# Kernel optimization log

Measured on AMD Instinct MI355X. Metric: run time of the kernel, lower is better.

## Reference

```python
import jax, jax.numpy as jnp
import numpy as np

HEADS = 8
DIM_HEAD = 64
SCALE = DIM_HEAD ** -0.5


def setup_inputs() -> dict:
    key = jax.random.key(0)
    ks = jax.random.split(key, 8)
    B, Nq, Dq = 4, 2048, 512
    Nk, Dc = 1024, 768
    inner = HEADS * DIM_HEAD  # 512
    x = jax.random.normal(ks[0], (B, Nq, Dq), dtype=jnp.float32)
    context = jax.random.normal(ks[1], (B, Nk, Dc), dtype=jnp.float32)
    # Linear weights stored [in, out]; y = x @ W (+ b)
    Wq = jax.random.normal(ks[2], (Dq, inner), dtype=jnp.float32) / np.sqrt(Dq)
    Wk = jax.random.normal(ks[3], (Dc, inner), dtype=jnp.float32) / np.sqrt(Dc)
    Wv = jax.random.normal(ks[4], (Dc, inner), dtype=jnp.float32) / np.sqrt(Dc)
    Wo = jax.random.normal(ks[5], (inner, Dq), dtype=jnp.float32) / np.sqrt(inner)
    bo = jax.random.normal(ks[6], (Dq,), dtype=jnp.float32) * 0.01
    return {"x": x, "context": context, "Wq": Wq, "Wk": Wk, "Wv": Wv, "Wo": Wo, "bo": bo}


def reference(x, context, Wq, Wk, Wv, Wo, bo):
    B, Nq, _ = x.shape
    Nk = context.shape[1]
    # projections
    q = x @ Wq          # [B, Nq, h*d]
    k = context @ Wk    # [B, Nk, h*d]
    v = context @ Wv    # [B, Nk, h*d]
    # split heads: b n (h d) -> b h n d
    q = q.reshape(B, Nq, HEADS, DIM_HEAD).transpose(0, 2, 1, 3)
    k = k.reshape(B, Nk, HEADS, DIM_HEAD).transpose(0, 2, 1, 3)
    v = v.reshape(B, Nk, HEADS, DIM_HEAD).transpose(0, 2, 1, 3)
    # fp32 QK^T (ATTN_PRECISION == 'fp32' path)
    sim = jnp.einsum('bhid,bhjd->bhij', q.astype(jnp.float32), k.astype(jnp.float32)) * SCALE
    attn = jax.nn.softmax(sim, axis=-1)
    out = jnp.einsum('bhij,bhjd->bhid', attn, v)  # [B, h, Nq, d]
    out = out.transpose(0, 2, 1, 3).reshape(B, Nq, HEADS * DIM_HEAD)
    return out @ Wo + bo  # dropout=0 -> identity
```

## Files before the change

kernel.cpp:

```cpp
#include <hip/hip_runtime.h>
#include <cstddef>
#include <cstdint>

typedef __attribute__((ext_vector_type(8))) short bf16x8;
typedef __attribute__((ext_vector_type(4))) float f32x4;

static __device__ __forceinline__ short f2bf(float f) {
    union { float f; unsigned u; } x;
    x.f = f;
    unsigned r = (x.u + 0x7FFFu + ((x.u >> 16) & 1u)) >> 16;
    return (short)r;
}

typedef __attribute__((address_space(3))) unsigned lds_u;
typedef const __attribute__((address_space(1))) unsigned glb_u;
static __device__ __forceinline__ void gld_lds16(const void* g, void* l) {
    __builtin_amdgcn_global_load_lds((glb_u*)g, (lds_u*)l, 16, 0, 0);
}

__global__ __launch_bounds__(256) void prep_kernel(
    const float* __restrict__ x, const float* __restrict__ c,
    short* __restrict__ xb, short* __restrict__ cb,
    const float* __restrict__ Wq, const float* __restrict__ Wk,
    const float* __restrict__ Wv, const float* __restrict__ Wo,
    short* __restrict__ wqT, short* __restrict__ wkvT, short* __restrict__ woT)
{
    __shared__ float T[32][33];
    const int bid = blockIdx.x;
    const int tid = threadIdx.x;
    if (bid < 7168) {
        int i = bid * 256 + tid;
        const float* src; short* dst; int off;
        if (i < 1048576) { src = x; dst = xb; off = i; }
        else { src = c; dst = cb; off = i - 1048576; }
        float4 v = ((const float4*)src)[off];
        ushort4 w;
        w.x = (unsigned short)f2bf(v.x); w.y = (unsigned short)f2bf(v.y);
        w.z = (unsigned short)f2bf(v.z); w.w = (unsigned short)f2bf(v.w);
        ((ushort4*)dst)[off] = w;
        return;
    }
    const int w0 = bid - 7168;
    const int z = w0 / 384, rem = w0 % 384;
    const int yt = rem >> 4, xt = rem & 15;
    const float* src; short* dst; int R;
    if (z == 0)      { src = Wq; dst = wqT;  R = 512; }
    else if (z == 1) { src = Wk; dst = wkvT; R = 768; }
    else if (z == 2) { src = Wv; dst = wkvT + (size_t)512 * 768; R = 768; }
    else             { src = Wo; dst = woT;  R = 512; }
    if (yt * 32 >= R) return;
    {
        int r = tid >> 3, c4 = (tid & 7) * 4;
        float4 v = *(const float4*)&src[(size_t)(yt * 32 + r) * 512 + xt * 32 + c4];
        T[r][c4] = v.x; T[r][c4 + 1] = v.y; T[r][c4 + 2] = v.z; T[r][c4 + 3] = v.w;
    }
    __syncthreads();
    {
        int cc = tid >> 3, r4 = (tid & 7) * 4;
        ushort4 w;
        w.x = (unsigned short)f2bf(T[r4][cc]);     w.y = (unsigned short)f2bf(T[r4 + 1][cc]);
        w.z = (unsigned short)f2bf(T[r4 + 2][cc]); w.w = (unsigned short)f2bf(T[r4 + 3][cc]);
        *(ushort4*)&dst[(size_t)(xt * 32 + cc) * R + yt * 32 + r4] = w;
    }
}

static __device__ __forceinline__ void gemm_core(
    const short* __restrict__ A, const short* __restrict__ BT, int K,
    int bm, int bn, short* As, short* Bs, f32x4 acc[4][4])
{
    const int tid  = threadIdx.x;
    const int lane = tid & 63;
    const int wave = tid >> 6;
    const int lm   = lane & 15;
    const int quad = lane >> 4;
    const int wm = (wave >> 1) * 64;
    const int wn = (wave & 1) * 64;
    const int c = tid >> 7, r = tid & 127;

    const short* Ag = &A[(size_t)(bm + r) * K + c * 8];
    const short* Bg = &BT[(size_t)(bn + r) * K + c * 8];

    gld_lds16(Ag,      &As[tid * 8]);
    gld_lds16(Ag + 16, &As[(tid + 256) * 8]);
    gld_lds16(Bg,      &Bs[tid * 8]);
    gld_lds16(Bg + 16, &Bs[(tid + 256) * 8]);
    Ag += 32; Bg += 32;
    gld_lds16(Ag,      &As[4096 + tid * 8]);
    gld_lds16(Ag + 16, &As[4096 + (tid + 256) * 8]);
    gld_lds16(Bg,      &Bs[4096 + tid * 8]);
    gld_lds16(Bg + 16, &Bs[4096 + (tid + 256) * 8]);
    Ag += 32; Bg += 32;

    const int NT = K >> 5;
    int ocur = 0;
    int onxt = 2 * 4096;
    for (int t = 0; t < NT; ++t) {
        if (t < NT - 1) asm volatile("s_waitcnt vmcnt(4)" ::: "memory");
        else            asm volatile("s_waitcnt vmcnt(0)" ::: "memory");
        __builtin_amdgcn_s_barrier();
        __builtin_amdgcn_sched_barrier(0);
        if (t < NT - 2) {
            gld_lds16(Ag,      &As[onxt + tid * 8]);
            gld_lds16(Ag + 16, &As[onxt + (tid + 256) * 8]);
            gld_lds16(Bg,      &Bs[onxt + tid * 8]);
            gld_lds16(Bg + 16, &Bs[onxt + (tid + 256) * 8]);
            Ag += 32; Bg += 32;
        }
        const short* Ac = As + ocur;
        const short* Bc = Bs + ocur;
        bf16x8 af[4], bfr[4];
        #pragma unroll
        for (int i = 0; i < 4; ++i)
            af[i] = *(const bf16x8*)&Ac[(quad * 128 + wm + i * 16 + lm) * 8];
        #pragma unroll
        for (int j = 0; j < 4; ++j)
            bfr[j] = *(const bf16x8*)&Bc[(quad * 128 + wn + j * 16 + lm) * 8];
        __builtin_amdgcn_s_setprio(1);
        #pragma unroll
        for (int i = 0; i < 4; ++i)
            #pragma unroll
            for (int j = 0; j < 4; ++j)
                acc[i][j] = __builtin_amdgcn_mfma_f32_16x16x32_bf16(
                    af[i], bfr[j], acc[i][j], 0, 0, 0);
        __builtin_amdgcn_s_setprio(0);
        ocur += 4096; if (ocur == 12288) ocur = 0;
        onxt += 4096; if (onxt == 12288) onxt = 0;
    }
}

__global__ __launch_bounds__(256) void qkv_kernel(
    const short* __restrict__ xb, const short* __restrict__ cb,
    const short* __restrict__ wqT, const short* __restrict__ wkvT,
    short* __restrict__ qb, short* __restrict__ kvb, short* __restrict__ vT)
{
    __shared__ short As[3 * 4096];
    __shared__ short Bs[3 * 4096];
    const int L = (blockIdx.x & 7) * 64 + (blockIdx.x >> 3);
    const short *A, *BT; int K, bm, bn;
    if (L < 256) { A = xb; BT = wqT;  K = 512; bm = (L >> 2) * 128; bn = (L & 3) * 128; }
    else { int b2 = L - 256; A = cb; BT = wkvT; K = 768;
           bm = (b2 >> 3) * 128; bn = (b2 & 7) * 128; }

    f32x4 acc[4][4] = {};
    gemm_core(A, BT, K, bm, bn, As, Bs, acc);

    const int lane = threadIdx.x & 63, wave = threadIdx.x >> 6;
    const int lm = lane & 15, quad = lane >> 4;
    const int wm = (wave >> 1) * 64, wn = (wave & 1) * 64;
    if (L < 256) {
        #pragma unroll
        for (int j = 0; j < 4; ++j) {
            int col = bn + wn + j * 16 + lm;
            #pragma unroll
            for (int i = 0; i < 4; ++i) {
                int row0 = bm + wm + i * 16 + quad * 4;
                #pragma unroll
                for (int r = 0; r < 4; ++r)
                    qb[(size_t)(row0 + r) * 512 + col] = f2bf(acc[i][j][r] * 0.18033688f);
            }
        }
    } else if (bn < 512) {
        #pragma unroll
        for (int j = 0; j < 4; ++j) {
            int col = bn + wn + j * 16 + lm;
            #pragma unroll
            for (int i = 0; i < 4; ++i) {
                int row0 = bm + wm + i * 16 + quad * 4;
                #pragma unroll
                for (int r = 0; r < 4; ++r)
                    kvb[(size_t)(row0 + r) * 1024 + col] = f2bf(acc[i][j][r]);
            }
        }
    } else {
        const int bq = bm >> 10;
        const int nbase = (bm & 1023) + wm;
        #pragma unroll
        for (int j = 0; j < 4; ++j) {
            int dimp = bn + wn + j * 16 + lm - 512;
            short* drow = &vT[((size_t)(bq * 512 + dimp)) * 1024];
            #pragma unroll
            for (int i = 0; i < 4; ++i) {
                int n0 = nbase + i * 16 + quad * 4;
                int nl = n0 & 63;
                int g  = ((nl >> 5) << 2) | ((nl >> 2) & 3);
                int p  = (n0 & ~63) | (g << 3) | (((nl >> 4) & 1) << 2);
                ushort4 w;
                w.x = (unsigned short)f2bf(acc[i][j][0]);
                w.y = (unsigned short)f2bf(acc[i][j][1]);
                w.z = (unsigned short)f2bf(acc[i][j][2]);
                w.w = (unsigned short)f2bf(acc[i][j][3]);
                *(ushort4*)&drow[p] = w;
            }
        }
    }
}

__global__ __launch_bounds__(256) void ogemm_kernel(
    const short* __restrict__ ob, const short* __restrict__ woT,
    const float* __restrict__ bias, float* __restrict__ out)
{
    __shared__ short As[3 * 4096];
    __shared__ short Bs[3 * 4096];
    const int L = (blockIdx.x & 7) * 32 + (blockIdx.x >> 3);
    const int bm = (L >> 2) * 128, bn = (L & 3) * 128;

    f32x4 acc[4][4] = {};
    gemm_core(ob, woT, 512, bm, bn, As, Bs, acc);

    const int lane = threadIdx.x & 63, wave = threadIdx.x >> 6;
    const int lm = lane & 15, quad = lane >> 4;
    const int wm = (wave >> 1) * 64, wn = (wave & 1) * 64;
    #pragma unroll
    for (int j = 0; j < 4; ++j) {
        int col = bn + wn + j * 16 + lm;
        float bv = bias[col];
        #pragma unroll
        for (int i = 0; i < 4; ++i) {
            int row0 = bm + wm + i * 16 + quad * 4;
            #pragma unroll
            for (int r = 0; r < 4; ++r)
                out[(size_t)(row0 + r) * 512 + col] = acc[i][j][r] + bv;
        }
    }
}

__global__ __launch_bounds__(256) void attn_kernel(
    const short* __restrict__ q, const short* __restrict__ k,
    const short* __restrict__ vT, short* __restrict__ o)
{
    __shared__ short Ks[2 * 8192];
    __shared__ short Vs[2 * 8192];

    const int tid  = threadIdx.x;
    const int lane = tid & 63;
    const int wave = tid >> 6;
    const int lm   = lane & 15;
    const int quad = lane >> 4;

    const int bid = blockIdx.x;
    const int xcdq = bid >> 3;
    const int hb = (bid & 7) + ((xcdq >> 4) << 3);
    const int qt = xcdq & 15;
    const int h = hb & 7, b = hb >> 3;

    const size_t qrow0 = (size_t)b * 2048 + qt * 128;
    const size_t krow0 = (size_t)b * 1024;
    const int hcol = h * 64;
    const size_t vrow0 = ((size_t)b * 8 + h) * 64;

    const int rk = tid & 127, ck = tid >> 7;
    const int dv = tid & 63,  nv = tid >> 6;
    const short* kg = &k[(krow0 + rk) * 1024 + hcol + ck * 8];
    const short* vg = &vT[(vrow0 + dv) * 1024 + nv * 8];

    #pragma unroll
    for (int c = 0; c < 4; ++c)
        gld_lds16(kg + c * 16, &Ks[((ck + 2 * c) * 128 + rk) * 8]);
    #pragma unroll
    for (int c = 0; c < 4; ++c)
        gld_lds16(vg + c * 32, &Vs[((nv + 4 * c) * 64 + dv) * 8]);
    kg += 128 * 1024; vg += 128;

    const short* qrow0p = &q[(qrow0 + wave * 32 + lm) * 512 + hcol];
    const short* qrow1p = qrow0p + 16 * 512;
    bf16x8 qf00 = *(const bf16x8*)&qrow0p[quad * 8];
    bf16x8 qf01 = *(const bf16x8*)&qrow0p[32 + quad * 8];
    bf16x8 qf10 = *(const bf16x8*)&qrow1p[quad * 8];
    bf16x8 qf11 = *(const bf16x8*)&qrow1p[32 + quad * 8];
    asm volatile("" :: "v"(qf00), "v"(qf01), "v"(qf10), "v"(qf11));

    f32x4 oacc[2][4] = {};
    float lsum[2] = {0.0f, 0.0f};
    const int frk = (quad * 128 + lm) * 8;
    const int frv = (quad * 64 + lm) * 8;

    for (int t = 0; t < 8; ++t) {
        asm volatile("s_waitcnt vmcnt(0)" ::: "memory");
        __builtin_amdgcn_s_barrier();
        __builtin_amdgcn_sched_barrier(0);
        const short* Kc = &Ks[(t & 1) * 8192];
        const short* Vc = &Vs[(t & 1) * 8192];
        if (t < 7) {
            short* Kn = &Ks[((t & 1) ^ 1) * 8192];
            short* Vn = &Vs[((t & 1) ^ 1) * 8192];
            #pragma unroll
            for (int c = 0; c < 4; ++c)
                gld_lds16(kg + c * 16, &Kn[((ck + 2 * c) * 128 + rk) * 8]);
            #pragma unroll
            for (int c = 0; c < 4; ++c)
                gld_lds16(vg + c * 32, &Vn[((nv + 4 * c) * 64 + dv) * 8]);
            kg += 128 * 1024; vg += 128;
        }

        f32x4 s0[8], s1[8];
        #pragma unroll
        for (int j = 0; j < 8; ++j) { s0[j] = (f32x4){}; s1[j] = (f32x4){}; }
        __builtin_amdgcn_s_setprio(1);
        #pragma unroll
        for (int j = 0; j < 8; ++j) {
            bf16x8 kf0 = *(const bf16x8*)&Kc[frk + j * 128];
            bf16x8 kf1 = *(const bf16x8*)&Kc[frk + 4096 + j * 128];
            s0[j] = __builtin_amdgcn_mfma_f32_16x16x32_bf16(kf0, qf00, s0[j], 0, 0, 0);
            s1[j] = __builtin_amdgcn_mfma_f32_16x16x32_bf16(kf0, qf10, s1[j], 0, 0, 0);
            s0[j] = __builtin_amdgcn_mfma_f32_16x16x32_bf16(kf1, qf01, s0[j], 0, 0, 0);
            s1[j] = __builtin_amdgcn_mfma_f32_16x16x32_bf16(kf1, qf11, s1[j], 0, 0, 0);
        }
        __builtin_amdgcn_s_setprio(0);

        union { unsigned u[4]; bf16x8 v; } pf0[4], pf1[4];
        #pragma unroll
        for (int j = 0; j < 8; ++j) {
            #pragma unroll
            for (int rp = 0; rp < 2; ++rp) {
                float a0 = __builtin_amdgcn_exp2f(s0[j][2 * rp]);
                float a1 = __builtin_amdgcn_exp2f(s0[j][2 * rp + 1]);
                float b0 = __builtin_amdgcn_exp2f(s1[j][2 * rp]);
                float b1 = __builtin_amdgcn_exp2f(s1[j][2 * rp + 1]);
                lsum[0] += a0 + a1;
                lsum[1] += b0 + b1;
                unsigned pa, pb;
                asm("v_cvt_pk_bf16_f32 %0, %1, %2" : "=v"(pa) : "v"(a0), "v"(a1));
                asm("v_cvt_pk_bf16_f32 %0, %1, %2" : "=v"(pb) : "v"(b0), "v"(b1));
                pf0[j >> 1].u[(j & 1) * 2 + rp] = pa;
                pf1[j >> 1].u[(j & 1) * 2 + rp] = pb;
            }
        }

        __builtin_amdgcn_s_setprio(1);
        #pragma unroll
        for (int jd = 0; jd < 4; ++jd) {
            #pragma unroll
            for (int s = 0; s < 4; ++s) {
                bf16x8 vf = *(const bf16x8*)&Vc[frv + s * 2048 + jd * 128];
                oacc[0][jd] = __builtin_amdgcn_mfma_f32_16x16x32_bf16(pf0[s].v, vf, oacc[0][jd], 0, 0, 0);
                oacc[1][jd] = __builtin_amdgcn_mfma_f32_16x16x32_bf16(pf1[s].v, vf, oacc[1][jd], 0, 0, 0);
            }
        }
        __builtin_amdgcn_s_setprio(0);
    }

    #pragma unroll
    for (int g = 0; g < 2; ++g) {
        float s = lsum[g];
        s += __shfl_xor(s, 16);
        s += __shfl_xor(s, 32);
        const float inv = 1.0f / s;
        float invr[4];
        #pragma unroll
        for (int r = 0; r < 4; ++r)
            invr[r] = __shfl(inv, quad * 20 + r);
        #pragma unroll
        for (int j = 0; j < 4; ++j) {
            int col = hcol + j * 16 + lm;
            #pragma unroll
            for (int r = 0; r < 4; ++r) {
                size_t row = qrow0 + wave * 32 + g * 16 + quad * 4 + r;
                o[row * 512 + col] = f2bf(oacc[g][j][r] * invr[r]);
            }
        }
    }
}

extern "C" void kernel_launch(void* const* d_in, const int* in_sizes, int n_in,
                              void* d_out, int out_size, void* d_ws, size_t ws_size,
                              hipStream_t stream)
{
    const float* x   = (const float*)d_in[0];
    const float* ctx = (const float*)d_in[1];
    const float* Wq  = (const float*)d_in[2];
    const float* Wk  = (const float*)d_in[3];
    const float* Wv  = (const float*)d_in[4];
    const float* Wo  = (const float*)d_in[5];
    const float* bo  = (const float*)d_in[6];

    char* ws = (char*)d_ws;
    short* xb   = (short*)(ws);
    short* cb   = (short*)(ws + (8u << 20));
    short* wqT  = (short*)(ws + (14u << 20));
    short* wkvT = (short*)(ws + (14u << 20) + (512u << 10));
    short* woT  = (short*)(ws + (16u << 20));
    short* qb   = (short*)(ws + (16u << 20) + (512u << 10));
    short* kvb  = (short*)(ws + (24u << 20) + (512u << 10));
    short* vT   = (short*)(ws + (33u << 20));
    short* ob   = xb;

    prep_kernel<<<8704, 256, 0, stream>>>(x, ctx, xb, cb, Wq, Wk, Wv, Wo, wqT, wkvT, woT);
    qkv_kernel<<<512, 256, 0, stream>>>(xb, cb, wqT, wkvT, qb, kvb, vT);
    attn_kernel<<<512, 256, 0, stream>>>(qb, kvb, vT, ob);
    ogemm_kernel<<<256, 256, 0, stream>>>(ob, woT, bo, (float*)d_out);
}
```

Before: 164.9 us.

## Fuse four kernels into one persistent kernel with atomic grid barriers

Replaces the prep, QKV-projection, attention and output-GEMM launches with a single 512-block kernel. The stages are separated by a software grid barrier built on an atomic counter, which is reset by a memset before launch. The goal is to remove launch overhead and the tail gaps between kernels. In exchange it needs all 512 blocks co-resident (launch_bounds 256,2 and 64KB of LDS), adds spin-wait costs, and has the prep stage loop inside each block.

```diff
diff --git a/kernel.cpp b/kernel.cpp
--- a/kernel.cpp
+++ b/kernel.cpp
@@ -18,50 +18,16 @@
     __builtin_amdgcn_global_load_lds((glb_u*)g, (lds_u*)l, 16, 0, 0);
 }
 
-__global__ __launch_bounds__(256) void prep_kernel(
-    const float* __restrict__ x, const float* __restrict__ c,
-    short* __restrict__ xb, short* __restrict__ cb,
-    const float* __restrict__ Wq, const float* __restrict__ Wk,
-    const float* __restrict__ Wv, const float* __restrict__ Wo,
-    short* __restrict__ wqT, short* __restrict__ wkvT, short* __restrict__ woT)
-{
-    __shared__ float T[32][33];
-    const int bid = blockIdx.x;
-    const int tid = threadIdx.x;
-    if (bid < 7168) {
-        int i = bid * 256 + tid;
-        const float* src; short* dst; int off;
-        if (i < 1048576) { src = x; dst = xb; off = i; }
-        else { src = c; dst = cb; off = i - 1048576; }
-        float4 v = ((const float4*)src)[off];
-        ushort4 w;
-        w.x = (unsigned short)f2bf(v.x); w.y = (unsigned short)f2bf(v.y);
-        w.z = (unsigned short)f2bf(v.z); w.w = (unsigned short)f2bf(v.w);
-        ((ushort4*)dst)[off] = w;
-        return;
-    }
-    const int w0 = bid - 7168;
-    const int z = w0 / 384, rem = w0 % 384;
-    const int yt = rem >> 4, xt = rem & 15;
-    const float* src; short* dst; int R;
-    if (z == 0)      { src = Wq; dst = wqT;  R = 512; }
-    else if (z == 1) { src = Wk; dst = wkvT; R = 768; }
-    else if (z == 2) { src = Wv; dst = wkvT + (size_t)512 * 768; R = 768; }
-    else             { src = Wo; dst = woT;  R = 512; }
-    if (yt * 32 >= R) return;
-    {
-        int r = tid >> 3, c4 = (tid & 7) * 4;
-        float4 v = *(const float4*)&src[(size_t)(yt * 32 + r) * 512 + xt * 32 + c4];
-        T[r][c4] = v.x; T[r][c4 + 1] = v.y; T[r][c4 + 2] = v.z; T[r][c4 + 3] = v.w;
-    }
+static __device__ __forceinline__ void gbar(unsigned* ctr, unsigned target) {
+    asm volatile("s_waitcnt vmcnt(0) lgkmcnt(0)" ::: "memory");
+    __threadfence();
     __syncthreads();
-    {
-        int cc = tid >> 3, r4 = (tid & 7) * 4;
-        ushort4 w;
-        w.x = (unsigned short)f2bf(T[r4][cc]);     w.y = (unsigned short)f2bf(T[r4 + 1][cc]);
-        w.z = (unsigned short)f2bf(T[r4 + 2][cc]); w.w = (unsigned short)f2bf(T[r4 + 3][cc]);
-        *(ushort4*)&dst[(size_t)(xt * 32 + cc) * R + yt * 32 + r4] = w;
-    }
+    if (threadIdx.x == 0) {
+        atomicAdd(ctr, 1u);
+        while (atomicAdd(ctr, 0u) < target) __builtin_amdgcn_s_sleep(8);
+    }
+    __syncthreads();
+    __threadfence();
 }
 
 static __device__ __forceinline__ void gemm_core(
@@ -128,234 +94,282 @@
     }
 }
 
-__global__ __launch_bounds__(256) void qkv_kernel(
-    const short* __restrict__ xb, const short* __restrict__ cb,
-    const short* __restrict__ wqT, const short* __restrict__ wkvT,
-    short* __restrict__ qb, short* __restrict__ kvb, short* __restrict__ vT)
+__global__ __launch_bounds__(256, 2) void mega_kernel(
+    const float* __restrict__ x, const float* __restrict__ ctx,
+    const float* __restrict__ Wq, const float* __restrict__ Wk,
+    const float* __restrict__ Wv, const float* __restrict__ Wo,
+    const float* __restrict__ bo,
+    short* __restrict__ xb, short* __restrict__ cb,
+    short* __restrict__ wqT, short* __restrict__ wkvT, short* __restrict__ woT,
+    short* __restrict__ qb, short* __restrict__ kvb, short* __restrict__ vT,
+    short* __restrict__ ob, float* __restrict__ out, unsigned* __restrict__ ctr)
 {
-    __shared__ short As[3 * 4096];
-    __shared__ short Bs[3 * 4096];
-    const int L = (blockIdx.x & 7) * 64 + (blockIdx.x >> 3);
-    const short *A, *BT; int K, bm, bn;
-    if (L < 256) { A = xb; BT = wqT;  K = 512; bm = (L >> 2) * 128; bn = (L & 3) * 128; }
-    else { int b2 = L - 256; A = cb; BT = wkvT; K = 768;
-           bm = (b2 >> 3) * 128; bn = (b2 & 7) * 128; }
-
-    f32x4 acc[4][4] = {};
-    gemm_core(A, BT, K, bm, bn, As, Bs, acc);
-
-    const int lane = threadIdx.x & 63, wave = threadIdx.x >> 6;
-    const int lm = lane & 15, quad = lane >> 4;
-    const int wm = (wave >> 1) * 64, wn = (wave & 1) * 64;
-    if (L < 256) {
+    __shared__ __align__(16) char SMEM[65536];
+    const int bid = blockIdx.x;
+    const int tid = threadIdx.x;
+
+    {
+        #pragma unroll 1
+        for (int it = 0; it < 14; ++it) {
+            int i = (bid + it * 512) * 256 + tid;
+            const float* src; short* dst; int off;
+            if (i < 1048576) { src = x; dst = xb; off = i; }
+            else { src = ctx; dst = cb; off = i - 1048576; }
+            float4 v = ((const float4*)src)[off];
+            ushort4 w;
+            w.x = (unsigned short)f2bf(v.x); w.y = (unsigned short)f2bf(v.y);
+            w.z = (unsigned short)f2bf(v.z); w.w = (unsigned short)f2bf(v.w);
+            ((ushort4*)dst)[off] = w;
+        }
+        float (*T)[33] = (float(*)[33])SMEM;
+        #pragma unroll 1
+        for (int it = 0; it < 3; ++it) {
+            int w0 = bid + it * 512;
+            int z = w0 / 384, rem = w0 % 384;
+            int yt = rem >> 4, xt = rem & 15;
+            const float* src; short* dst; int R;
+            if (z == 0)      { src = Wq; dst = wqT;  R = 512; }
+            else if (z == 1) { src = Wk; dst = wkvT; R = 768; }
+            else if (z == 2) { src = Wv; dst = wkvT + (size_t)512 * 768; R = 768; }
+            else             { src = Wo; dst = woT;  R = 512; }
+            const bool act = (yt * 32 < R);
+            if (act) {
+                int r = tid >> 3, c4 = (tid & 7) * 4;
+                float4 v = *(const float4*)&src[(size_t)(yt * 32 + r) * 512 + xt * 32 + c4];
+                T[r][c4] = v.x; T[r][c4 + 1] = v.y; T[r][c4 + 2] = v.z; T[r][c4 + 3] = v.w;
+            }
+            __syncthreads();
+            if (act) {
+                int cc = tid >> 3, r4 = (tid & 7) * 4;
+                ushort4 w;
+                w.x = (unsigned short)f2bf(T[r4][cc]);     w.y = (unsigned short)f2bf(T[r4 + 1][cc]);
+                w.z = (unsigned short)f2bf(T[r4 + 2][cc]); w.w = (unsigned short)f2bf(T[r4 + 3][cc]);
+                *(ushort4*)&dst[(size_t)(xt * 32 + cc) * R + yt * 32 + r4] = w;
+            }
+            __syncthreads();
+        }
+    }
+    gbar(ctr, 512);
+
+    {
+        short* As = (short*)SMEM;
+        short* Bs = (short*)(SMEM + 24576);
+        const int L = (bid & 7) * 64 + (bid >> 3);
+        const short *A, *BT; int K, bm, bn;
+        if (L < 256) { A = xb; BT = wqT;  K = 512; bm = (L >> 2) * 128; bn = (L & 3) * 128; }
+        else { int b2 = L - 256; A = cb; BT = wkvT; K = 768;
+               bm = (b2 >> 3) * 128; bn = (b2 & 7) * 128; }
+
+        f32x4 acc[4][4] = {};
+        gemm_core(A, BT, K, bm, bn, As, Bs, acc);
+
+        const int lane = tid & 63, wave = tid >> 6;
+        const int lm = lane & 15, quad = lane >> 4;
+        const int wm = (wave >> 1) * 64, wn = (wave & 1) * 64;
+        if (L < 256) {
+            #pragma unroll
+            for (int j = 0; j < 4; ++j) {
+                int col = bn + wn + j * 16 + lm;
+                #pragma unroll
+                for (int i = 0; i < 4; ++i) {
+                    int row0 = bm + wm + i * 16 + quad * 4;
+                    #pragma unroll
+                    for (int r = 0; r < 4; ++r)
+                        qb[(size_t)(row0 + r) * 512 + col] = f2bf(acc[i][j][r] * 0.18033688f);
+                }
+            }
+        } else if (bn < 512) {
+            #pragma unroll
+            for (int j = 0; j < 4; ++j) {
+                int col = bn + wn + j * 16 + lm;
+                #pragma unroll
+                for (int i = 0; i < 4; ++i) {
+                    int row0 = bm + wm + i * 16 + quad * 4;
+                    #pragma unroll
+                    for (int r = 0; r < 4; ++r)
+                        kvb[(size_t)(row0 + r) * 1024 + col] = f2bf(acc[i][j][r]);
+                }
+            }
+        } else {
+            const int bq = bm >> 10;
+            const int nbase = (bm & 1023) + wm;
+            #pragma unroll
+            for (int j = 0; j < 4; ++j) {
+                int dimp = bn + wn + j * 16 + lm - 512;
+                short* drow = &vT[((size_t)(bq * 512 + dimp)) * 1024];
+                #pragma unroll
+                for (int i = 0; i < 4; ++i) {
+                    int n0 = nbase + i * 16 + quad * 4;
+                    int nl = n0 & 63;
+                    int g  = ((nl >> 5) << 2) | ((nl >> 2) & 3);
+                    int p  = (n0 & ~63) | (g << 3) | (((nl >> 4) & 1) << 2);
+                    ushort4 w;
+                    w.x = (unsigned short)f2bf(acc[i][j][0]);
+                    w.y = (unsigned short)f2bf(acc[i][j][1]);
+                    w.z = (unsigned short)f2bf(acc[i][j][2]);
+                    w.w = (unsigned short)f2bf(acc[i][j][3]);
+                    *(ushort4*)&drow[p] = w;
+                }
+            }
+        }
+    }
+    gbar(ctr, 1024);
+
+    {
+        short* Ks = (short*)SMEM;
+        short* Vs = (short*)(SMEM + 32768);
+        const int lane = tid & 63;
+        const int wave = tid >> 6;
+        const int lm   = lane & 15;
+        const int quad = lane >> 4;
+
+        const int xcdq = bid >> 3;
+        const int hb = (bid & 7) + ((xcdq >> 4) << 3);
+        const int qt = xcdq & 15;
+        const int h = hb & 7, b = hb >> 3;
+
+        const size_t qrow0 = (size_t)b * 2048 + qt * 128;
+        const size_t krow0 = (size_t)b * 1024;
+        const int hcol = h * 64;
+        const size_t vrow0 = ((size_t)b * 8 + h) * 64;
+
+        const int rk = tid & 127, ck = tid >> 7;
+        const int dv = tid & 63,  nv = tid >> 6;
+        const short* kg = &kvb[(krow0 + rk) * 1024 + hcol + ck * 8];
+        const short* vg = &vT[(vrow0 + dv) * 1024 + nv * 8];
+
+        #pragma unroll
+        for (int c = 0; c < 4; ++c)
+            gld_lds16(kg + c * 16, &Ks[((ck + 2 * c) * 128 + rk) * 8]);
+        #pragma unroll
+        for (int c = 0; c < 4; ++c)
+            gld_lds16(vg + c * 32, &Vs[((nv + 4 * c) * 64 + dv) * 8]);
+        kg += 128 * 1024; vg += 128;
+
+        const short* qrow0p = &qb[(qrow0 + wave * 32 + lm) * 512 + hcol];
+        const short* qrow1p = qrow0p + 16 * 512;
+        bf16x8 qf00 = *(const bf16x8*)&qrow0p[quad * 8];
+        bf16x8 qf01 = *(const bf16x8*)&qrow0p[32 + quad * 8];
+        bf16x8 qf10 = *(const bf16x8*)&qrow1p[quad * 8];
+        bf16x8 qf11 = *(const bf16x8*)&qrow1p[32 + quad * 8];
+        asm volatile("" :: "v"(qf00), "v"(qf01), "v"(qf10), "v"(qf11));
+
+        f32x4 oacc[2][4] = {};
+        float lsum[2] = {0.0f, 0.0f};
+        const int frk = (quad * 128 + lm) * 8;
+        const int frv = (quad * 64 + lm) * 8;
+
+        for (int t = 0; t < 8; ++t) {
+            asm volatile("s_waitcnt vmcnt(0)" ::: "memory");
+            __builtin_amdgcn_s_barrier();
+            __builtin_amdgcn_sched_barrier(0);
+            const short* Kc = &Ks[(t & 1) * 8192];
+            const short* Vc = &Vs[(t & 1) * 8192];
+            if (t < 7) {
+                short* Kn = &Ks[((t & 1) ^ 1) * 8192];
+                short* Vn = &Vs[((t & 1) ^ 1) * 8192];
+                #pragma unroll
+                for (int c = 0; c < 4; ++c)
+                    gld_lds16(kg + c * 16, &Kn[((ck + 2 * c) * 128 + rk) * 8]);
+                #pragma unroll
+                for (int c = 0; c < 4; ++c)
+                    gld_lds16(vg + c * 32, &Vn[((nv + 4 * c) * 64 + dv) * 8]);
+                kg += 128 * 1024; vg += 128;
+            }
+
+            f32x4 s0[8], s1[8];
+            #pragma unroll
+            for (int j = 0; j < 8; ++j) { s0[j] = (f32x4){}; s1[j] = (f32x4){}; }
+            __builtin_amdgcn_s_setprio(1);
+            #pragma unroll
+            for (int j = 0; j < 8; ++j) {
+                bf16x8 kf0 = *(const bf16x8*)&Kc[frk + j * 128];
+                bf16x8 kf1 = *(const bf16x8*)&Kc[frk + 4096 + j * 128];
+                s0[j] = __builtin_amdgcn_mfma_f32_16x16x32_bf16(kf0, qf00, s0[j], 0, 0, 0);
+                s1[j] = __builtin_amdgcn_mfma_f32_16x16x32_bf16(kf0, qf10, s1[j], 0, 0, 0);
+                s0[j] = __builtin_amdgcn_mfma_f32_16x16x32_bf16(kf1, qf01, s0[j], 0, 0, 0);
+                s1[j] = __builtin_amdgcn_mfma_f32_16x16x32_bf16(kf1, qf11, s1[j], 0, 0, 0);
+            }
+            __builtin_amdgcn_s_setprio(0);
+
+            union { unsigned u[4]; bf16x8 v; } pf0[4], pf1[4];
+            #pragma unroll
+            for (int j = 0; j < 8; ++j) {
+                #pragma unroll
+                for (int rp = 0; rp < 2; ++rp) {
+                    float a0 = __builtin_amdgcn_exp2f(s0[j][2 * rp]);
+                    float a1 = __builtin_amdgcn_exp2f(s0[j][2 * rp + 1]);
+                    float b0 = __builtin_amdgcn_exp2f(s1[j][2 * rp]);
+                    float b1 = __builtin_amdgcn_exp2f(s1[j][2 * rp + 1]);
+                    lsum[0] += a0 + a1;
+                    lsum[1] += b0 + b1;
+                    unsigned pa, pb;
+                    asm("v_cvt_pk_bf16_f32 %0, %1, %2" : "=v"(pa) : "v"(a0), "v"(a1));
+                    asm("v_cvt_pk_bf16_f32 %0, %1, %2" : "=v"(pb) : "v"(b0), "v"(b1));
+                    pf0[j >> 1].u[(j & 1) * 2 + rp] = pa;
+                    pf1[j >> 1].u[(j & 1) * 2 + rp] = pb;
+                }
+            }
+
+            __builtin_amdgcn_s_setprio(1);
+            #pragma unroll
+            for (int jd = 0; jd < 4; ++jd) {
+                #pragma unroll
+                for (int s = 0; s < 4; ++s) {
+                    bf16x8 vf = *(const bf16x8*)&Vc[frv + s * 2048 + jd * 128];
+                    oacc[0][jd] = __builtin_amdgcn_mfma_f32_16x16x32_bf16(pf0[s].v, vf, oacc[0][jd], 0, 0, 0);
+                    oacc[1][jd] = __builtin_amdgcn_mfma_f32_16x16x32_bf16(pf1[s].v, vf, oacc[1][jd], 0, 0, 0);
+                }
+            }
+            __builtin_amdgcn_s_setprio(0);
+        }
+
+        #pragma unroll
+        for (int g = 0; g < 2; ++g) {
+            float s = lsum[g];
+            s += __shfl_xor(s, 16);
+            s += __shfl_xor(s, 32);
+            const float inv = 1.0f / s;
+            float invr[4];
+            #pragma unroll
+            for (int r = 0; r < 4; ++r)
+                invr[r] = __shfl(inv, quad * 20 + r);
+            #pragma unroll
+            for (int j = 0; j < 4; ++j) {
+                int col = hcol + j * 16 + lm;
+                #pragma unroll
+                for (int r = 0; r < 4; ++r) {
+                    size_t row = qrow0 + wave * 32 + g * 16 + quad * 4 + r;
+                    ob[row * 512 + col] = f2bf(oacc[g][j][r] * invr[r]);
+                }
+            }
+        }
+    }
+    gbar(ctr, 1536);
+
+    if (bid >= 256) return;
+    {
+        short* As = (short*)SMEM;
+        short* Bs = (short*)(SMEM + 24576);
+        const int L = (bid & 7) * 32 + (bid >> 3);
+        const int bm = (L >> 2) * 128, bn = (L & 3) * 128;
+
+        f32x4 acc[4][4] = {};
+        gemm_core(ob, woT, 512, bm, bn, As, Bs, acc);
+
+        const int lane = tid & 63, wave = tid >> 6;
+        const int lm = lane & 15, quad = lane >> 4;
+        const int wm = (wave >> 1) * 64, wn = (wave & 1) * 64;
         #pragma unroll
         for (int j = 0; j < 4; ++j) {
             int col = bn + wn + j * 16 + lm;
+            float bv = bo[col];
             #pragma unroll
             for (int i = 0; i < 4; ++i) {
                 int row0 = bm + wm + i * 16 + quad * 4;
                 #pragma unroll
                 for (int r = 0; r < 4; ++r)
-                    qb[(size_t)(row0 + r) * 512 + col] = f2bf(acc[i][j][r] * 0.18033688f);
-            }
-        }
-    } else if (bn < 512) {
-        #pragma unroll
-        for (int j = 0; j < 4; ++j) {
-            int col = bn + wn + j * 16 + lm;
-            #pragma unroll
-            for (int i = 0; i < 4; ++i) {
-                int row0 = bm + wm + i * 16 + quad * 4;
-                #pragma unroll
-                for (int r = 0; r < 4; ++r)
-                    kvb[(size_t)(row0 + r) * 1024 + col] = f2bf(acc[i][j][r]);
-            }
-        }
-    } else {
-        const int bq = bm >> 10;
-        const int nbase = (bm & 1023) + wm;
-        #pragma unroll
-        for (int j = 0; j < 4; ++j) {
-            int dimp = bn + wn + j * 16 + lm - 512;
-            short* drow = &vT[((size_t)(bq * 512 + dimp)) * 1024];
-            #pragma unroll
-            for (int i = 0; i < 4; ++i) {
-                int n0 = nbase + i * 16 + quad * 4;
-                int nl = n0 & 63;
-                int g  = ((nl >> 5) << 2) | ((nl >> 2) & 3);
-                int p  = (n0 & ~63) | (g << 3) | (((nl >> 4) & 1) << 2);
-                ushort4 w;
-                w.x = (unsigned short)f2bf(acc[i][j][0]);
-                w.y = (unsigned short)f2bf(acc[i][j][1]);
-                w.z = (unsigned short)f2bf(acc[i][j][2]);
-                w.w = (unsigned short)f2bf(acc[i][j][3]);
-                *(ushort4*)&drow[p] = w;
-            }
-        }
-    }
-}
-
-__global__ __launch_bounds__(256) void ogemm_kernel(
-    const short* __restrict__ ob, const short* __restrict__ woT,
-    const float* __restrict__ bias, float* __restrict__ out)
-{
-    __shared__ short As[3 * 4096];
-    __shared__ short Bs[3 * 4096];
-    const int L = (blockIdx.x & 7) * 32 + (blockIdx.x >> 3);
-    const int bm = (L >> 2) * 128, bn = (L & 3) * 128;
-
-    f32x4 acc[4][4] = {};
-    gemm_core(ob, woT, 512, bm, bn, As, Bs, acc);
-
-    const int lane = threadIdx.x & 63, wave = threadIdx.x >> 6;
-    const int lm = lane & 15, quad = lane >> 4;
-    const int wm = (wave >> 1) * 64, wn = (wave & 1) * 64;
-    #pragma unroll
-    for (int j = 0; j < 4; ++j) {
-        int col = bn + wn + j * 16 + lm;
-        float bv = bias[col];
-        #pragma unroll
-        for (int i = 0; i < 4; ++i) {
-            int row0 = bm + wm + i * 16 + quad * 4;
-            #pragma unroll
-            for (int r = 0; r < 4; ++r)
-                out[(size_t)(row0 + r) * 512 + col] = acc[i][j][r] + bv;
-        }
-    }
-}
-
-__global__ __launch_bounds__(256) void attn_kernel(
-    const short* __restrict__ q, const short* __restrict__ k,
-    const short* __restrict__ vT, short* __restrict__ o)
-{
-    __shared__ short Ks[2 * 8192];
-    __shared__ short Vs[2 * 8192];
-
-    const int tid  = threadIdx.x;
-    const int lane = tid & 63;
-    const int wave = tid >> 6;
-    const int lm   = lane & 15;
-    const int quad = lane >> 4;
-
-    const int bid = blockIdx.x;
-    const int xcdq = bid >> 3;
-    const int hb = (bid & 7) + ((xcdq >> 4) << 3);
-    const int qt = xcdq & 15;
-    const int h = hb & 7, b = hb >> 3;
-
-    const size_t qrow0 = (size_t)b * 2048 + qt * 128;
-    const size_t krow0 = (size_t)b * 1024;
-    const int hcol = h * 64;
-    const size_t vrow0 = ((size_t)b * 8 + h) * 64;
-
-    const int rk = tid & 127, ck = tid >> 7;
-    const int dv = tid & 63,  nv = tid >> 6;
-    const short* kg = &k[(krow0 + rk) * 1024 + hcol + ck * 8];
-    const short* vg = &vT[(vrow0 + dv) * 1024 + nv * 8];
-
-    #pragma unroll
-    for (int c = 0; c < 4; ++c)
-        gld_lds16(kg + c * 16, &Ks[((ck + 2 * c) * 128 + rk) * 8]);
-    #pragma unroll
-    for (int c = 0; c < 4; ++c)
-        gld_lds16(vg + c * 32, &Vs[((nv + 4 * c) * 64 + dv) * 8]);
-    kg += 128 * 1024; vg += 128;
-
-    const short* qrow0p = &q[(qrow0 + wave * 32 + lm) * 512 + hcol];
-    const short* qrow1p = qrow0p + 16 * 512;
-    bf16x8 qf00 = *(const bf16x8*)&qrow0p[quad * 8];
-    bf16x8 qf01 = *(const bf16x8*)&qrow0p[32 + quad * 8];
-    bf16x8 qf10 = *(const bf16x8*)&qrow1p[quad * 8];
-    bf16x8 qf11 = *(const bf16x8*)&qrow1p[32 + quad * 8];
-    asm volatile("" :: "v"(qf00), "v"(qf01), "v"(qf10), "v"(qf11));
-
-    f32x4 oacc[2][4] = {};
-    float lsum[2] = {0.0f, 0.0f};
-    const int frk = (quad * 128 + lm) * 8;
-    const int frv = (quad * 64 + lm) * 8;
-
-    for (int t = 0; t < 8; ++t) {
-        asm volatile("s_waitcnt vmcnt(0)" ::: "memory");
-        __builtin_amdgcn_s_barrier();
-        __builtin_amdgcn_sched_barrier(0);
-        const short* Kc = &Ks[(t & 1) * 8192];
-        const short* Vc = &Vs[(t & 1) * 8192];
-        if (t < 7) {
-            short* Kn = &Ks[((t & 1) ^ 1) * 8192];
-            short* Vn = &Vs[((t & 1) ^ 1) * 8192];
-            #pragma unroll
-            for (int c = 0; c < 4; ++c)
-                gld_lds16(kg + c * 16, &Kn[((ck + 2 * c) * 128 + rk) * 8]);
-            #pragma unroll
-            for (int c = 0; c < 4; ++c)
-                gld_lds16(vg + c * 32, &Vn[((nv + 4 * c) * 64 + dv) * 8]);
-            kg += 128 * 1024; vg += 128;
-        }
-
-        f32x4 s0[8], s1[8];
-        #pragma unroll
-        for (int j = 0; j < 8; ++j) { s0[j] = (f32x4){}; s1[j] = (f32x4){}; }
-        __builtin_amdgcn_s_setprio(1);
-        #pragma unroll
-        for (int j = 0; j < 8; ++j) {
-            bf16x8 kf0 = *(const bf16x8*)&Kc[frk + j * 128];
-            bf16x8 kf1 = *(const bf16x8*)&Kc[frk + 4096 + j * 128];
-            s0[j] = __builtin_amdgcn_mfma_f32_16x16x32_bf16(kf0, qf00, s0[j], 0, 0, 0);
-            s1[j] = __builtin_amdgcn_mfma_f32_16x16x32_bf16(kf0, qf10, s1[j], 0, 0, 0);
-            s0[j] = __builtin_amdgcn_mfma_f32_16x16x32_bf16(kf1, qf01, s0[j], 0, 0, 0);
-            s1[j] = __builtin_amdgcn_mfma_f32_16x16x32_bf16(kf1, qf11, s1[j], 0, 0, 0);
-        }
-        __builtin_amdgcn_s_setprio(0);
-
-        union { unsigned u[4]; bf16x8 v; } pf0[4], pf1[4];
-        #pragma unroll
-        for (int j = 0; j < 8; ++j) {
-            #pragma unroll
-            for (int rp = 0; rp < 2; ++rp) {
-                float a0 = __builtin_amdgcn_exp2f(s0[j][2 * rp]);
-                float a1 = __builtin_amdgcn_exp2f(s0[j][2 * rp + 1]);
-                float b0 = __builtin_amdgcn_exp2f(s1[j][2 * rp]);
-                float b1 = __builtin_amdgcn_exp2f(s1[j][2 * rp + 1]);
-                lsum[0] += a0 + a1;
-                lsum[1] += b0 + b1;
-                unsigned pa, pb;
-                asm("v_cvt_pk_bf16_f32 %0, %1, %2" : "=v"(pa) : "v"(a0), "v"(a1));
-                asm("v_cvt_pk_bf16_f32 %0, %1, %2" : "=v"(pb) : "v"(b0), "v"(b1));
-                pf0[j >> 1].u[(j & 1) * 2 + rp] = pa;
-                pf1[j >> 1].u[(j & 1) * 2 + rp] = pb;
-            }
-        }
-
-        __builtin_amdgcn_s_setprio(1);
-        #pragma unroll
-        for (int jd = 0; jd < 4; ++jd) {
-            #pragma unroll
-            for (int s = 0; s < 4; ++s) {
-                bf16x8 vf = *(const bf16x8*)&Vc[frv + s * 2048 + jd * 128];
-                oacc[0][jd] = __builtin_amdgcn_mfma_f32_16x16x32_bf16(pf0[s].v, vf, oacc[0][jd], 0, 0, 0);
-                oacc[1][jd] = __builtin_amdgcn_mfma_f32_16x16x32_bf16(pf1[s].v, vf, oacc[1][jd], 0, 0, 0);
-            }
-        }
-        __builtin_amdgcn_s_setprio(0);
-    }
-
-    #pragma unroll
-    for (int g = 0; g < 2; ++g) {
-        float s = lsum[g];
-        s += __shfl_xor(s, 16);
-        s += __shfl_xor(s, 32);
-        const float inv = 1.0f / s;
-        float invr[4];
-        #pragma unroll
-        for (int r = 0; r < 4; ++r)
-            invr[r] = __shfl(inv, quad * 20 + r);
-        #pragma unroll
-        for (int j = 0; j < 4; ++j) {
-            int col = hcol + j * 16 + lm;
-            #pragma unroll
-            for (int r = 0; r < 4; ++r) {
-                size_t row = qrow0 + wave * 32 + g * 16 + quad * 4 + r;
-                o[row * 512 + col] = f2bf(oacc[g][j][r] * invr[r]);
+                    out[(size_t)(row0 + r) * 512 + col] = acc[i][j][r] + bv;
             }
         }
     }
@@ -382,10 +396,12 @@
     short* qb   = (short*)(ws + (16u << 20) + (512u << 10));
     short* kvb  = (short*)(ws + (24u << 20) + (512u << 10));
     short* vT   = (short*)(ws + (33u << 20));
-    short* ob   = xb;
-
-    prep_kernel<<<8704, 256, 0, stream>>>(x, ctx, xb, cb, Wq, Wk, Wv, Wo, wqT, wkvT, woT);
-    qkv_kernel<<<512, 256, 0, stream>>>(xb, cb, wqT, wkvT, qb, kvb, vT);
-    attn_kernel<<<512, 256, 0, stream>>>(qb, kvb, vT, ob);
-    ogemm_kernel<<<256, 256, 0, stream>>>(ob, woT, bo, (float*)d_out);
-}
+    short* ob   = (short*)(ws + (38u << 20));
+    unsigned* ctr = (unsigned*)(ws + (48u << 20));
+    float* outp = (float*)d_out;
+
+    hipMemsetAsync(ctr, 0, 4, stream);
+    mega_kernel<<<512, 256, 0, stream>>>(
+        x, ctx, Wq, Wk, Wv, Wo, bo, xb, cb, wqT, wkvT, woT,
+        qb, kvb, vT, ob, outp, ctr);
+}
```

New measurement: 494.6 us. 200% more time.
